# Kernel tuning notes

Measured on AMD Instinct MI355X. Metric: run time of the kernel, lower is better.

## Reference

```python
import jax, jax.numpy as jnp
import numpy as np

L, B, S, D, F, H = 4, 2, 1024, 1024, 4096, 16
EPS = 1e-5


def setup_inputs() -> dict:
    key = jax.random.key(0)
    ks = jax.random.split(key, 15)
    w = lambda k, shape, s=0.02: (jax.random.normal(k, shape, jnp.float32) * s)
    inp = {
        "x": jax.random.normal(ks[0], (B, S, D), jnp.float32),
        # stacked per-layer params (scanned over leading L axis)
        "ln1_w": jnp.ones((L, D), jnp.float32),
        "ln1_b": jnp.zeros((L, D), jnp.float32),
        "Wq": w(ks[1], (L, D, D)),
        "Wk": w(ks[2], (L, D, D)),
        "Wv": w(ks[3], (L, D, D)),
        "Wo": w(ks[4], (L, D, D)),
        "bo": jnp.zeros((L, D), jnp.float32),
        "ln2_w": jnp.ones((L, D), jnp.float32),
        "ln2_b": jnp.zeros((L, D), jnp.float32),
        "W1": w(ks[5], (L, D, F)),
        "b1": jnp.zeros((L, F), jnp.float32),
        "W2": w(ks[6], (L, F, D)),
        "b2": jnp.zeros((L, D), jnp.float32),
    }
    return inp


def _layernorm(y, w, b):
    m = jnp.mean(y, axis=-1, keepdims=True)
    v = jnp.mean(jnp.square(y - m), axis=-1, keepdims=True)
    return (y - m) * jax.lax.rsqrt(v + EPS) * w + b


def _block(x, p):
    ln1w, ln1b, wq, wk, wv, wo, bo, ln2w, ln2b, w1, b1, w2, b2 = p
    b, s, d = x.shape
    dh = d // H
    scale = dh ** -0.5
    # --- attention sub-block (pre-norm, residual) ---
    h = _layernorm(x, ln1w, ln1b)
    q = (h @ wq).reshape(b, s, H, dh).transpose(0, 2, 1, 3)  # bhsd
    k = (h @ wk).reshape(b, s, H, dh).transpose(0, 2, 1, 3)
    v = (h @ wv).reshape(b, s, H, dh).transpose(0, 2, 1, 3)
    attn = jax.nn.softmax(jnp.einsum("bhqd,bhkd->bhqk", q, k) * scale, axis=-1)
    o = jnp.einsum("bhqk,bhkd->bhqd", attn, v).transpose(0, 2, 1, 3).reshape(b, s, d)
    x = x + (o @ wo + bo)
    # --- FFN sub-block (pre-norm, residual) ---
    h = _layernorm(x, ln2w, ln2b)
    x = x + (jax.nn.gelu(h @ w1 + b1, approximate=False) @ w2 + b2)
    return x, None


def reference(x, ln1_w, ln1_b, Wq, Wk, Wv, Wo, bo, ln2_w, ln2_b, W1, b1, W2, b2):
    xs = (ln1_w, ln1_b, Wq, Wk, Wv, Wo, bo, ln2_w, ln2_b, W1, b1, W2, b2)
    out, _ = jax.lax.scan(_block, x, xs)
    return out
```

## Files before the change

### kernel.cpp

```cpp
#include <hip/hip_runtime.h>
#include <hip/hip_bf16.h>

using bf16   = __bf16;
using bf16x2 = __attribute__((ext_vector_type(2))) __bf16;
using bf16x4 = __attribute__((ext_vector_type(4))) __bf16;
using bf16x8 = __attribute__((ext_vector_type(8))) __bf16;
using f32x4  = __attribute__((ext_vector_type(4))) float;

constexpr int LAYERS = 4;
constexpr int BATCH  = 2;
constexpr int SEQ    = 1024;
constexpr int DIM    = 1024;
constexpr int FF     = 4096;
constexpr int HEADS  = 16;
constexpr int TOK    = BATCH * SEQ;
constexpr int QKVN   = 3 * DIM;
constexpr float EPS  = 1e-5f;

__device__ __forceinline__ void gload_lds16(const void* g, void* l) {
    __builtin_amdgcn_global_load_lds(
        (const __attribute__((address_space(1))) void*)g,
        (__attribute__((address_space(3))) void*)l, 16, 0, 0);
}

__global__ __launch_bounds__(256) void ln_kernel(
    const float* __restrict__ x, const float* __restrict__ g,
    const float* __restrict__ bt, bf16* __restrict__ out)
{
    __shared__ float red[8];
    const int row = blockIdx.x, t = threadIdx.x;
    const float4 v = ((const float4*)(x + (size_t)row * DIM))[t];

    float s = v.x + v.y + v.z + v.w;
    #pragma unroll
    for (int o = 32; o; o >>= 1) s += __shfl_down(s, o, 64);
    if ((t & 63) == 0) red[t >> 6] = s;
    __syncthreads();
    const float mean = (red[0] + red[1] + red[2] + red[3]) * (1.0f / DIM);

    const float dx = v.x - mean, dy = v.y - mean, dz = v.z - mean, dw = v.w - mean;
    float q = dx * dx + dy * dy + dz * dz + dw * dw;
    #pragma unroll
    for (int o = 32; o; o >>= 1) q += __shfl_down(q, o, 64);
    if ((t & 63) == 0) red[4 + (t >> 6)] = q;
    __syncthreads();
    const float var = (red[4] + red[5] + red[6] + red[7]) * (1.0f / DIM);
    const float rstd = rsqrtf(var + EPS);

    const float4 gg = ((const float4*)g)[t];
    const float4 bb = ((const float4*)bt)[t];
    bf16x4 o4;
    o4[0] = (bf16)(dx * rstd * gg.x + bb.x);
    o4[1] = (bf16)(dy * rstd * gg.y + bb.y);
    o4[2] = (bf16)(dz * rstd * gg.z + bb.z);
    o4[3] = (bf16)(dw * rstd * gg.w + bb.w);
    *(bf16x4*)(out + (size_t)row * DIM + t * 4) = o4;
}

template<bool DO_LN>
__global__ __launch_bounds__(256) void lncomb_kernel(
    float* __restrict__ x, const bf16* __restrict__ p,
    const float* __restrict__ bias, const float* __restrict__ g,
    const float* __restrict__ bt, bf16* __restrict__ out)
{
    __shared__ float red[8];
    const int row = blockIdx.x, t = threadIdx.x;
    float4 v = ((const float4*)(x + (size_t)row * DIM))[t];
    const float4 bv = ((const float4*)bias)[t];
    float a0 = bv.x, a1 = bv.y, a2 = bv.z, a3 = bv.w;
    #pragma unroll
    for (int ks = 0; ks < 4; ++ks) {
        const bf16x4 pp = *(const bf16x4*)(p + (size_t)(ks * TOK + row) * DIM + t * 4);
        a0 += (float)pp[0]; a1 += (float)pp[1];
        a2 += (float)pp[2]; a3 += (float)pp[3];
    }
    v.x += a0; v.y += a1; v.z += a2; v.w += a3;
    ((float4*)(x + (size_t)row * DIM))[t] = v;
    if (!DO_LN) return;

    float s = v.x + v.y + v.z + v.w;
    #pragma unroll
    for (int o = 32; o; o >>= 1) s += __shfl_down(s, o, 64);
    if ((t & 63) == 0) red[t >> 6] = s;
    __syncthreads();
    const float mean = (red[0] + red[1] + red[2] + red[3]) * (1.0f / DIM);

    const float dx = v.x - mean, dy = v.y - mean, dz = v.z - mean, dw = v.w - mean;
    float q = dx * dx + dy * dy + dz * dz + dw * dw;
    #pragma unroll
    for (int o = 32; o; o >>= 1) q += __shfl_down(q, o, 64);
    if ((t & 63) == 0) red[4 + (t >> 6)] = q;
    __syncthreads();
    const float var = (red[4] + red[5] + red[6] + red[7]) * (1.0f / DIM);
    const float rstd = rsqrtf(var + EPS);

    const float4 gg = ((const float4*)g)[t];
    const float4 bb = ((const float4*)bt)[t];
    bf16x4 o4;
    o4[0] = (bf16)(dx * rstd * gg.x + bb.x);
    o4[1] = (bf16)(dy * rstd * gg.y + bb.y);
    o4[2] = (bf16)(dz * rstd * gg.z + bb.z);
    o4[3] = (bf16)(dw * rstd * gg.w + bb.w);
    *(bf16x4*)(out + (size_t)row * DIM + t * 4) = o4;
}

__global__ __launch_bounds__(256) void wtrans_all_kernel(
    const float* __restrict__ Wq, const float* __restrict__ Wk,
    const float* __restrict__ Wv, const float* __restrict__ Wo,
    const float* __restrict__ W1, const float* __restrict__ W2,
    bf16* __restrict__ wqkvt, bf16* __restrict__ wot,
    bf16* __restrict__ w1t, bf16* __restrict__ w2t)
{
    __shared__ float tile[64][65];
    const int bid = blockIdx.x;
    const float* W; bf16* Wt; int N, K, rowoff, bx, by;
    if (bid < 768) {
        const int seg = bid >> 8, r = bid & 255;
        W = (seg == 0) ? Wq : (seg == 1) ? Wk : Wv;
        Wt = wqkvt; N = DIM; K = DIM; rowoff = seg * DIM;
        bx = r & 15; by = r >> 4;
    } else if (bid < 1024) {
        const int r = bid - 768;
        W = Wo; Wt = wot; N = DIM; K = DIM; rowoff = 0;
        bx = r & 15; by = r >> 4;
    } else if (bid < 2048) {
        const int r = bid - 1024;
        W = W1; Wt = w1t; N = FF; K = DIM; rowoff = 0;
        bx = r & 63; by = r >> 6;
    } else {
        const int r = bid - 2048;
        W = W2; Wt = w2t; N = DIM; K = FF; rowoff = 0;
        bx = r & 15; by = r >> 4;
    }
    const int bn = bx * 64, bk = by * 64;
    {
        const int r16 = threadIdx.x >> 4, c4 = (threadIdx.x & 15) * 4;
        #pragma unroll
        for (int i = 0; i < 4; ++i) {
            const int kr = r16 + i * 16;
            const float4 v = *(const float4*)(W + (size_t)(bk + kr) * N + bn + c4);
            tile[kr][c4 + 0] = v.x; tile[kr][c4 + 1] = v.y;
            tile[kr][c4 + 2] = v.z; tile[kr][c4 + 3] = v.w;
        }
    }
    __syncthreads();
    {
        const int n = threadIdx.x >> 2, ch = threadIdx.x & 3;
        #pragma unroll
        for (int i = 0; i < 2; ++i) {
            const int k0 = (ch + i * 4) * 8;
            bf16x8 o;
            #pragma unroll
            for (int j = 0; j < 8; ++j) o[j] = (bf16)tile[k0 + j][n];
            *(bf16x8*)(Wt + (size_t)(rowoff + bn + n) * K + bk + k0) = o;
        }
    }
}

template<int EPI, int SK>
__global__ __launch_bounds__(256) void gemm_kernel(
    const bf16* __restrict__ A, const bf16* __restrict__ Bt,
    const float* __restrict__ bias, void* __restrict__ outv,
    int M, int N, int Kfull)
{
    constexpr int MR = 2;
    __shared__ bf16 As[2][128 * 32];
    __shared__ bf16 Bs[2][64 * 32];

    const int t    = threadIdx.x;
    const int lane = t & 63;
    const int w    = t >> 6;
    const int wm   = w * 32;
    const int kg   = lane >> 4, lr = lane & 15;
    const int key  = (lr >> 1) & 3;

    const int nwg = gridDim.x;
    const int bid = (blockIdx.x & 7) * (nwg >> 3) + (blockIdx.x >> 3);
    const int nbn = N / 64, nbm = M / 128;
    const int ks  = (SK > 1) ? bid / (nbm * nbn) : 0;
    const int r   = (SK > 1) ? bid % (nbm * nbn) : bid;
    const int bm  = ((SK > 1) ? (r / nbn) : (r % nbm)) * 128;
    const int bn  = ((SK > 1) ? (r % nbn) : (r / nbm)) * 64;

    const int Ksl = Kfull / SK;
    const int kof = ks * Ksl;

    f32x4 acc[MR][4] = {};

    auto stage = [&](int buf, int k0) {
        #pragma unroll
        for (int it = 0; it < 2; ++it) {
            const int ci = it * 256 + t, row = ci >> 2, c = ci & 3;
            gload_lds16(A + (size_t)(bm + row) * Kfull + kof + k0 + ((c ^ ((row >> 1) & 3)) << 3),
                        &As[buf][ci * 8]);
        }
        {
            const int ci = t, row = ci >> 2, c = ci & 3;
            gload_lds16(Bt + (size_t)(bn + row) * Kfull + kof + k0 + ((c ^ ((row >> 1) & 3)) << 3),
                        &Bs[buf][ci * 8]);
        }
    };

    stage(0, 0);
    __syncthreads();

    int cur = 0;
    for (int k0 = 0; k0 < Ksl; k0 += 32) {
        if (k0 + 32 < Ksl) stage(cur ^ 1, k0 + 32);

        bf16x8 af[MR], bfr[4];
        #pragma unroll
        for (int m = 0; m < MR; ++m) {
            const int row = wm + m * 16 + lr;
            af[m] = *(const bf16x8*)(&As[cur][row * 32 + ((kg ^ key) << 3)]);
        }
        #pragma unroll
        for (int n = 0; n < 4; ++n) {
            const int row = n * 16 + lr;
            bfr[n] = *(const bf16x8*)(&Bs[cur][row * 32 + ((kg ^ key) << 3)]);
        }
        #pragma unroll
        for (int m = 0; m < MR; ++m)
            #pragma unroll
            for (int n = 0; n < 4; ++n)
                acc[m][n] = __builtin_amdgcn_mfma_f32_16x16x32_bf16(af[m], bfr[n], acc[m][n], 0, 0, 0);

        __syncthreads();
        cur ^= 1;
    }

    #pragma unroll
    for (int m = 0; m < MR; ++m) {
        const int row = bm + wm + m * 16 + kg * 4;
        #pragma unroll
        for (int n = 0; n < 4; ++n) {
            const int col = bn + n * 16 + lr;
            #pragma unroll
            for (int j = 0; j < 4; ++j) {
                const float vv = acc[m][n][j];
                const size_t idx = (size_t)(row + j) * N + col;
                if (EPI == 0) {
                    ((bf16*)outv)[idx] = (bf16)vv;
                } else if (EPI == 1) {
                    const float z = vv + bias[col];
                    const float gl = 0.5f * z * (1.0f + erff(z * 0.70710678118654752f));
                    ((bf16*)outv)[idx] = (bf16)gl;
                } else {
                    ((bf16*)outv)[(size_t)ks * M * N + idx] = (bf16)vv;
                }
            }
        }
    }
}

__global__ __launch_bounds__(256) void attn_kernel(
    const bf16* __restrict__ qkv, bf16* __restrict__ od)
{
    __shared__ bf16 Ks[2][64 * 64];
    __shared__ bf16 Vt[2][64][64];
    __shared__ bf16 Ps[4][16][72];

    const int nwg = gridDim.x;
    const int bid = (blockIdx.x & 7) * (nwg >> 3) + (blockIdx.x >> 3);
    const int q0  = (bid & 15) * 64;
    const int bh  = bid >> 4;
    const int b   = bh >> 4, h = bh & 15;
    const int t   = threadIdx.x, w = t >> 6, lane = t & 63;
    const int kg  = lane >> 4, lr = lane & 15;

    const bf16* qbase = qkv + (size_t)b * SEQ * QKVN + h * 64;
    const bf16* kbase = qbase + DIM;
    const bf16* vbase = qbase + 2 * DIM;

    bf16x8 qf0, qf1;
    {
        const bf16* qr = qbase + (size_t)(q0 + w * 16 + lr) * QKVN;
        qf0 = *(const bf16x8*)(qr + kg * 8);
        qf1 = *(const bf16x8*)(qr + 32 + kg * 8);
        #pragma unroll
        for (int j = 0; j < 8; ++j) {
            qf0[j] = (bf16)((float)qf0[j] * 0.125f);
            qf1[j] = (bf16)((float)qf1[j] * 0.125f);
        }
    }

    f32x4 o_acc[4] = {};
    float m_run = -1e30f, l_run = 0.f;

    const int rp = t >> 3, cV = t & 7;

    bf16x8 vr0, vr1;
    auto loadV = [&](int kb) {
        vr0 = *(const bf16x8*)(vbase + (size_t)(kb + 2 * rp) * QKVN + cV * 8);
        vr1 = *(const bf16x8*)(vbase + (size_t)(kb + 2 * rp + 1) * QKVN + cV * 8);
    };
    auto stageK = [&](int buf, int kb) {
        #pragma unroll
        for (int i = 0; i < 2; ++i) {
            const int ci = i * 256 + t, row = ci >> 3, c = ci & 7;
            gload_lds16(kbase + (size_t)(kb + row) * QKVN + ((c ^ (row & 7)) << 3),
                        &Ks[buf][ci * 8]);
        }
    };
    auto storeV = [&](int buf) {
        #pragma unroll
        for (int j = 0; j < 8; ++j) {
            bf16x2 p; p[0] = vr0[j]; p[1] = vr1[j];
            const int d  = cV * 8 + j;
            const int dw = (((rp >> 2) ^ (j ^ cV)) << 2) | (rp & 3);
            *(bf16x2*)((char*)&Vt[buf][d][0] + dw * 4) = p;
        }
    };

    loadV(0);
    stageK(0, 0);
    storeV(0);
    __syncthreads();

    int cur = 0;
    for (int kb = 0; kb < SEQ; kb += 64) {
        const bool more = (kb + 64 < SEQ);
        if (more) { loadV(kb + 64); stageK(cur ^ 1, kb + 64); }

        f32x4 s[4] = {};
        __builtin_amdgcn_s_setprio(1);
        #pragma unroll
        for (int n = 0; n < 4; ++n) {
            const int row = n * 16 + lr;
            const bf16x8 kf0 = *(const bf16x8*)&Ks[cur][row * 64 + ((kg ^ (lr & 7)) << 3)];
            const bf16x8 kf1 = *(const bf16x8*)&Ks[cur][row * 64 + (((4 + kg) ^ (lr & 7)) << 3)];
            s[n] = __builtin_amdgcn_mfma_f32_16x16x32_bf16(kf0, qf0, s[n], 0, 0, 0);
            s[n] = __builtin_amdgcn_mfma_f32_16x16x32_bf16(kf1, qf1, s[n], 0, 0, 0);
        }
        __builtin_amdgcn_s_setprio(0);

        float pmax = -1e30f;
        #pragma unroll
        for (int n = 0; n < 4; ++n)
            #pragma unroll
            for (int j = 0; j < 4; ++j) pmax = fmaxf(pmax, s[n][j]);
        pmax = fmaxf(pmax, __shfl_xor(pmax, 16, 64));
        pmax = fmaxf(pmax, __shfl_xor(pmax, 32, 64));

        if (!__all(pmax <= m_run + 8.0f)) {
            const float mn   = fmaxf(m_run, pmax);
            const float corr = __expf(m_run - mn);
            m_run = mn;
            l_run *= corr;
            #pragma unroll
            for (int nd = 0; nd < 4; ++nd)
                #pragma unroll
                for (int j = 0; j < 4; ++j) o_acc[nd][j] *= corr;
        }

        float rs = 0.f;
        #pragma unroll
        for (int n = 0; n < 4; ++n)
            #pragma unroll
            for (int j = 0; j < 4; ++j) {
                const float e = __expf(s[n][j] - m_run);
                s[n][j] = e; rs += e;
            }
        rs += __shfl_xor(rs, 16, 64);
        rs += __shfl_xor(rs, 32, 64);
        l_run += rs;

        #pragma unroll
        for (int n = 0; n < 4; ++n) {
            bf16x4 pw;
            #pragma unroll
            for (int j = 0; j < 4; ++j) pw[j] = (bf16)s[n][j];
            *(bf16x4*)&Ps[w][lr][n * 16 + kg * 4] = pw;
        }

        const bf16x8 pf0 = *(const bf16x8*)&Ps[w][lr][kg * 8];
        const bf16x8 pf1 = *(const bf16x8*)&Ps[w][lr][32 + kg * 8];
        __builtin_amdgcn_s_setprio(1);
        #pragma unroll
        for (int nd = 0; nd < 4; ++nd) {
            const int d   = nd * 16 + lr;
            const int keyv = (d ^ (d >> 3)) & 7;
            const bf16x8 vf0 = *(const bf16x8*)((const char*)&Vt[cur][d][0] + ((kg ^ keyv) << 4));
            const bf16x8 vf1 = *(const bf16x8*)((const char*)&Vt[cur][d][0] + (((4 + kg) ^ keyv) << 4));
            o_acc[nd] = __builtin_amdgcn_mfma_f32_16x16x32_bf16(vf0, pf0, o_acc[nd], 0, 0, 0);
            o_acc[nd] = __builtin_amdgcn_mfma_f32_16x16x32_bf16(vf1, pf1, o_acc[nd], 0, 0, 0);
        }
        __builtin_amdgcn_s_setprio(0);

        if (more) storeV(cur ^ 1);
        __syncthreads();
        cur ^= 1;
    }

    const float inv = 1.0f / l_run;
    bf16* ob = od + (size_t)(b * SEQ + q0 + w * 16 + lr) * DIM + h * 64;
    #pragma unroll
    for (int nd = 0; nd < 4; ++nd) {
        bf16x4 o4;
        #pragma unroll
        for (int j = 0; j < 4; ++j) o4[j] = (bf16)(o_acc[nd][j] * inv);
        *(bf16x4*)(ob + nd * 16 + kg * 4) = o4;
    }
}

extern "C" void kernel_launch(void* const* d_in, const int* in_sizes, int n_in,
                              void* d_out, int out_size, void* d_ws, size_t ws_size,
                              hipStream_t stream)
{
    const float* x    = (const float*)d_in[0];
    const float* ln1w = (const float*)d_in[1];
    const float* ln1b = (const float*)d_in[2];
    const float* Wq   = (const float*)d_in[3];
    const float* Wk   = (const float*)d_in[4];
    const float* Wv   = (const float*)d_in[5];
    const float* Wo   = (const float*)d_in[6];
    const float* bo   = (const float*)d_in[7];
    const float* ln2w = (const float*)d_in[8];
    const float* ln2b = (const float*)d_in[9];
    const float* W1   = (const float*)d_in[10];
    const float* b1   = (const float*)d_in[11];
    const float* W2   = (const float*)d_in[12];
    const float* b2   = (const float*)d_in[13];

    char* ws = (char*)d_ws;
    float* xbuf  = (float*)(ws);
    bf16*  hbuf  = (bf16*)(ws + (8ull  << 20));
    bf16*  qkvb  = (bf16*)(ws + (12ull << 20));
    bf16*  obuf  = (bf16*)(ws + (24ull << 20));
    bf16*  gbuf  = (bf16*)(ws + (28ull << 20));
    bf16*  wqkvt = (bf16*)(ws + (44ull << 20));
    bf16*  wot   = (bf16*)(ws + (50ull << 20));
    bf16*  w1t   = (bf16*)(ws + (52ull << 20));
    bf16*  w2t   = (bf16*)(ws + (60ull << 20));
    bf16*  pbuf  = (bf16*)(ws + (68ull << 20));

    hipMemcpyAsync(xbuf, x, (size_t)TOK * DIM * sizeof(float),
                   hipMemcpyDeviceToDevice, stream);

    const size_t DD = (size_t)DIM * DIM, DF = (size_t)DIM * FF;
    for (int l = 0; l < LAYERS; ++l) {
        wtrans_all_kernel<<<3072, 256, 0, stream>>>(
            Wq + l * DD, Wk + l * DD, Wv + l * DD, Wo + l * DD,
            W1 + l * DF, W2 + l * DF, wqkvt, wot, w1t, w2t);

        if (l == 0)
            ln_kernel<<<TOK, 256, 0, stream>>>(xbuf, ln1w, ln1b, hbuf);

        gemm_kernel<0, 1><<<16 * 48, 256, 0, stream>>>(
            hbuf, wqkvt, nullptr, qkvb, TOK, QKVN, DIM);

        attn_kernel<<<512, 256, 0, stream>>>(qkvb, obuf);

        gemm_kernel<3, 4><<<16 * 16 * 4, 256, 0, stream>>>(
            obuf, wot, nullptr, pbuf, TOK, DIM, DIM);

        lncomb_kernel<true><<<TOK, 256, 0, stream>>>(
            xbuf, pbuf, bo + l * DIM, ln2w + l * DIM, ln2b + l * DIM, hbuf);

        gemm_kernel<1, 1><<<16 * 64, 256, 0, stream>>>(
            hbuf, w1t, b1 + l * FF, gbuf, TOK, FF, DIM);

        gemm_kernel<3, 4><<<16 * 16 * 4, 256, 0, stream>>>(
            gbuf, w2t, nullptr, pbuf, TOK, DIM, FF);

        if (l + 1 < LAYERS)
            lncomb_kernel<true><<<TOK, 256, 0, stream>>>(
                xbuf, pbuf, b2 + l * DIM, ln1w + (l + 1) * DIM, ln1b + (l + 1) * DIM, hbuf);
        else
            lncomb_kernel<false><<<TOK, 256, 0, stream>>>(
                xbuf, pbuf, b2 + l * DIM, nullptr, nullptr, nullptr);
    }

    hipMemcpyAsync(d_out, xbuf, (size_t)TOK * DIM * sizeof(float),
                   hipMemcpyDeviceToDevice, stream);
}
```

Before: 606.8 us.

## Add 128x128x64 GEMM tile kernel for QKV, FFN1 and FFN2 projections

Adds a new GEMM kernel with 128x128 output tiles and a K-step of 64. Each of the four waves computes a 64x64 sub-tile with 4x4 MFMA accumulators, and the LDS layout is XOR-swizzled. The QKV, W1 and W2 GEMMs switch to this kernel with fewer workgroups, while the Wo GEMM keeps the old 128x64 kernel. The larger tiles raise operand reuse and cut global and LDS traffic per FLOP, at the cost of more registers and LDS, lower occupancy and fewer blocks (W2 drops to 512 workgroups).

Measured after the change: 586.1 us. 3.4% less time.

```diff
diff --git a/kernel.cpp b/kernel.cpp
--- a/kernel.cpp
+++ b/kernel.cpp
@@ -158,7 +158,107 @@
 }
 
 template<int EPI, int SK>
-__global__ __launch_bounds__(256) void gemm_kernel(
+__global__ __launch_bounds__(256) void gemm128_kernel(
+    const bf16* __restrict__ A, const bf16* __restrict__ Bt,
+    const float* __restrict__ bias, void* __restrict__ outv,
+    int M, int N, int Kfull)
+{
+    __shared__ bf16 As[2][128 * 64];
+    __shared__ bf16 Bs[2][128 * 64];
+
+    const int t    = threadIdx.x;
+    const int lane = t & 63;
+    const int w    = t >> 6;
+    const int wm   = (w >> 1) * 64;
+    const int wn   = (w & 1) * 64;
+    const int kg   = lane >> 4, lr = lane & 15;
+    const int key  = lr & 7;
+
+    const int nwg = gridDim.x;
+    const int bid = (blockIdx.x & 7) * (nwg >> 3) + (blockIdx.x >> 3);
+    const int nbn = N / 128, nbm = M / 128;
+    const int ks  = (SK > 1) ? bid / (nbm * nbn) : 0;
+    const int r   = (SK > 1) ? bid % (nbm * nbn) : bid;
+    const int bm  = ((SK > 1) ? (r / nbn) : (r % nbm)) * 128;
+    const int bn  = ((SK > 1) ? (r % nbn) : (r / nbm)) * 128;
+
+    const int Ksl = Kfull / SK;
+    const int kof = ks * Ksl;
+
+    f32x4 acc[4][4] = {};
+
+    auto stage = [&](int buf, int k0) {
+        #pragma unroll
+        for (int it = 0; it < 4; ++it) {
+            const int ci = it * 256 + t, row = ci >> 3, c = ci & 7;
+            gload_lds16(A + (size_t)(bm + row) * Kfull + kof + k0 + ((c ^ (row & 7)) << 3),
+                        &As[buf][ci * 8]);
+        }
+        #pragma unroll
+        for (int it = 0; it < 4; ++it) {
+            const int ci = it * 256 + t, row = ci >> 3, c = ci & 7;
+            gload_lds16(Bt + (size_t)(bn + row) * Kfull + kof + k0 + ((c ^ (row & 7)) << 3),
+                        &Bs[buf][ci * 8]);
+        }
+    };
+
+    stage(0, 0);
+    __syncthreads();
+
+    int cur = 0;
+    for (int k0 = 0; k0 < Ksl; k0 += 64) {
+        if (k0 + 64 < Ksl) stage(cur ^ 1, k0 + 64);
+
+        #pragma unroll
+        for (int kk = 0; kk < 2; ++kk) {
+            bf16x8 af[4], bfr[4];
+            #pragma unroll
+            for (int m = 0; m < 4; ++m) {
+                const int row = wm + m * 16 + lr;
+                af[m] = *(const bf16x8*)(&As[cur][row * 64 + (((kk * 4 + kg) ^ key) << 3)]);
+            }
+            #pragma unroll
+            for (int n = 0; n < 4; ++n) {
+                const int row = wn + n * 16 + lr;
+                bfr[n] = *(const bf16x8*)(&Bs[cur][row * 64 + (((kk * 4 + kg) ^ key) << 3)]);
+            }
+            #pragma unroll
+            for (int m = 0; m < 4; ++m)
+                #pragma unroll
+                for (int n = 0; n < 4; ++n)
+                    acc[m][n] = __builtin_amdgcn_mfma_f32_16x16x32_bf16(af[m], bfr[n], acc[m][n], 0, 0, 0);
+        }
+
+        __syncthreads();
+        cur ^= 1;
+    }
+
+    #pragma unroll
+    for (int m = 0; m < 4; ++m) {
+        const int row = bm + wm + m * 16 + kg * 4;
+        #pragma unroll
+        for (int n = 0; n < 4; ++n) {
+            const int col = bn + wn + n * 16 + lr;
+            #pragma unroll
+            for (int j = 0; j < 4; ++j) {
+                const float vv = acc[m][n][j];
+                const size_t idx = (size_t)(row + j) * N + col;
+                if (EPI == 0) {
+                    ((bf16*)outv)[idx] = (bf16)vv;
+                } else if (EPI == 1) {
+                    const float z = vv + bias[col];
+                    const float gl = 0.5f * z * (1.0f + erff(z * 0.70710678118654752f));
+                    ((bf16*)outv)[idx] = (bf16)gl;
+                } else {
+                    ((bf16*)outv)[(size_t)ks * M * N + idx] = (bf16)vv;
+                }
+            }
+        }
+    }
+}
+
+template<int EPI, int SK>
+__global__ __launch_bounds__(256) void gemm64_kernel(
     const bf16* __restrict__ A, const bf16* __restrict__ Bt,
     const float* __restrict__ bias, void* __restrict__ outv,
     int M, int N, int Kfull)
@@ -446,21 +546,21 @@
         if (l == 0)
             ln_kernel<<<TOK, 256, 0, stream>>>(xbuf, ln1w, ln1b, hbuf);
 
-        gemm_kernel<0, 1><<<16 * 48, 256, 0, stream>>>(
+        gemm128_kernel<0, 1><<<16 * 24, 256, 0, stream>>>(
             hbuf, wqkvt, nullptr, qkvb, TOK, QKVN, DIM);
 
         attn_kernel<<<512, 256, 0, stream>>>(qkvb, obuf);
 
-        gemm_kernel<3, 4><<<16 * 16 * 4, 256, 0, stream>>>(
+        gemm64_kernel<3, 4><<<16 * 16 * 4, 256, 0, stream>>>(
             obuf, wot, nullptr, pbuf, TOK, DIM, DIM);
 
         lncomb_kernel<true><<<TOK, 256, 0, stream>>>(
             xbuf, pbuf, bo + l * DIM, ln2w + l * DIM, ln2b + l * DIM, hbuf);
 
-        gemm_kernel<1, 1><<<16 * 64, 256, 0, stream>>>(
+        gemm128_kernel<1, 1><<<16 * 32, 256, 0, stream>>>(
             hbuf, w1t, b1 + l * FF, gbuf, TOK, FF, DIM);
 
-        gemm_kernel<3, 4><<<16 * 16 * 4, 256, 0, stream>>>(
+        gemm128_kernel<3, 4><<<16 * 8 * 4, 256, 0, stream>>>(
             gbuf, w2t, nullptr, pbuf, TOK, DIM, FF);
 
         if (l + 1 < LAYERS)
```
